# Performance work log

Measured on AMD Instinct MI355X. Metric: run time of the kernel, lower is better.

Reference implementation:

```python
import jax, jax.numpy as jnp
import numpy as np

ALPHA = 1.0

def setup_inputs() -> dict:
    key = jax.random.key(0)
    k1, k2 = jax.random.split(key)
    x = jax.random.normal(k1, (65536, 256), dtype=jnp.float32)
    clusters = jax.random.normal(k2, (512, 256), dtype=jnp.float32)
    return {"x": x, "clusters": clusters}

def reference(x, clusters):
    # squared L2 distance without materializing [B, K, D] broadcasts:
    # d[b,k] = |x_b|^2 + |c_k|^2 - 2 x_b . c_k
    x_sq = jnp.sum(x * x, axis=1, keepdims=True)            # [B, 1]
    c_sq = jnp.sum(clusters * clusters, axis=1)[None, :]    # [1, K]
    cross = jnp.einsum('bd,kd->bk', x, clusters)            # [B, K]
    d = x_sq + c_sq - 2.0 * cross                           # [B, K]
    # Student-t kernel soft assignment
    q = (1.0 + d / ALPHA) ** (-(ALPHA + 1.0) / 2.0)
    q = q / jnp.sum(q, axis=1, keepdims=True)
    return q
```

## Files before the change

kernel.cpp:

```cpp
#include <hip/hip_runtime.h>
#include <hip/hip_bf16.h>

typedef __attribute__((ext_vector_type(8))) short bf16x8;
typedef __attribute__((ext_vector_type(4))) float f32x4;

#define K_DIM 256
#define N_DIM 512
#define BM 32
#define M_DIM 65536

__device__ __forceinline__ unsigned short f2bf(float f) {
    unsigned int u = __float_as_uint(f);
    unsigned int r = (u + 0x7fffu + ((u >> 16) & 1u)) >> 16;
    return (unsigned short)r;
}

__device__ __forceinline__ void gload_lds16(const unsigned short* g, unsigned short* l) {
    __builtin_amdgcn_global_load_lds(
        (const __attribute__((address_space(1))) void*)g,
        (__attribute__((address_space(3))) void*)l, 16, 0, 0);
}

__global__ __launch_bounds__(256) void prep_clusters(
        const float* __restrict__ clusters,
        unsigned short* __restrict__ cba,
        float* __restrict__ csq) {
    const int row = blockIdx.x;
    const int t = threadIdx.x;
    const float v = clusters[row * K_DIM + t];
    const int wc = row >> 6, n = (row >> 4) & 3, r = row & 15;
    const int ks = t >> 5, kh = (t >> 3) & 3, ko = t & 7;
    cba[(size_t)wc * 16384 + ks * 2048 + n * 512 + (kh * 16 + r) * 8 + ko] = f2bf(v);
    float s = v * v;
    #pragma unroll
    for (int m = 1; m < 64; m <<= 1) s += __shfl_xor(s, m);
    __shared__ float red[4];
    if ((t & 63) == 0) red[t >> 6] = s;
    __syncthreads();
    if (t == 0) csq[row] = red[0] + red[1] + red[2] + red[3];
}

__global__ __launch_bounds__(512, 6) void cluster_q(
        const float* __restrict__ x,
        const unsigned short* __restrict__ cba,
        const float* __restrict__ csq,
        float* __restrict__ out) {
    __shared__ __align__(16) unsigned short xa[BM * K_DIM];
    __shared__ __align__(16) unsigned short bB[8 * 2048];
    __shared__ float xsq[BM];
    __shared__ __align__(16) float csql[N_DIM];
    __shared__ float rsum[8][BM];

    const int t = threadIdx.x;
    const int lane = t & 63;
    const int wc = t >> 6;
    const int rowbase = blockIdx.x * BM;

    unsigned short* myB = bB + wc * 2048;
    const unsigned short* gsrc = cba + (size_t)wc * 16384;

    #pragma unroll
    for (int n = 0; n < 4; ++n)
        gload_lds16(gsrc + n * 512 + lane * 8, myB + n * 512);

    if (t < N_DIM) csql[t] = csq[t];

    #pragma unroll
    for (int p = 0; p < 4; ++p) {
        const int row = wc + p * 8;
        const float4 v = reinterpret_cast<const float4*>(
                             x + (size_t)(rowbase + row) * K_DIM)[lane];
        float s = v.x * v.x + v.y * v.y + v.z * v.z + v.w * v.w;
        #pragma unroll
        for (int m = 1; m < 64; m <<= 1) s += __shfl_xor(s, m);
        if (lane == 0) xsq[row] = s;
        const ushort4 pk = make_ushort4(f2bf(v.x), f2bf(v.y), f2bf(v.z), f2bf(v.w));
        const int swz = (lane * 8) ^ ((row & 7) << 4);
        *reinterpret_cast<ushort4*>(reinterpret_cast<char*>(xa) + row * 512 + swz) = pk;
    }
    __syncthreads();

    f32x4 acc[2][4];
    #pragma unroll
    for (int m = 0; m < 2; ++m)
        #pragma unroll
        for (int n = 0; n < 4; ++n)
            acc[m][n] = (f32x4){0.f, 0.f, 0.f, 0.f};

    #pragma unroll
    for (int ks = 0; ks < 8; ++ks) {
        asm volatile("s_waitcnt vmcnt(0)" ::: "memory");
        __builtin_amdgcn_sched_barrier(0);
        bf16x8 a[4];
        #pragma unroll
        for (int n = 0; n < 4; ++n)
            a[n] = *reinterpret_cast<const bf16x8*>(myB + n * 512 + lane * 8);
        const int r0 = (lane & 15);
        const int r1 = 16 + (lane & 15);
        const int c0 = (ks * 64 + (lane >> 4) * 16) ^ ((r0 & 7) << 4);
        const int c1 = (ks * 64 + (lane >> 4) * 16) ^ ((r1 & 7) << 4);
        const bf16x8 xm0 = *reinterpret_cast<const bf16x8*>(
                               reinterpret_cast<const char*>(xa) + r0 * 512 + c0);
        const bf16x8 xm1 = *reinterpret_cast<const bf16x8*>(
                               reinterpret_cast<const char*>(xa) + r1 * 512 + c1);
        asm volatile("s_waitcnt lgkmcnt(0)" ::: "memory");
        __builtin_amdgcn_sched_barrier(0);
        if (ks < 7) {
            #pragma unroll
            for (int n = 0; n < 4; ++n)
                gload_lds16(gsrc + (ks + 1) * 2048 + n * 512 + lane * 8,
                            myB + n * 512);
        }
        __builtin_amdgcn_sched_barrier(0);
        #pragma unroll
        for (int n = 0; n < 4; ++n) {
            acc[0][n] = __builtin_amdgcn_mfma_f32_16x16x32_bf16(a[n], xm0, acc[0][n], 0, 0, 0);
            acc[1][n] = __builtin_amdgcn_mfma_f32_16x16x32_bf16(a[n], xm1, acc[1][n], 0, 0, 0);
        }
    }

    const float4* csql4 = reinterpret_cast<const float4*>(csql);
    float part[2] = {0.f, 0.f};
    #pragma unroll
    for (int m = 0; m < 2; ++m) {
        const float xs1 = 1.f + xsq[m * 16 + (lane & 15)];
        #pragma unroll
        for (int n = 0; n < 4; ++n) {
            const float4 cs = csql4[wc * 16 + n * 4 + (lane >> 4)];
            f32x4 q;
            q[0] = __builtin_amdgcn_rcpf(fmaf(-2.f, acc[m][n][0], xs1 + cs.x));
            q[1] = __builtin_amdgcn_rcpf(fmaf(-2.f, acc[m][n][1], xs1 + cs.y));
            q[2] = __builtin_amdgcn_rcpf(fmaf(-2.f, acc[m][n][2], xs1 + cs.z));
            q[3] = __builtin_amdgcn_rcpf(fmaf(-2.f, acc[m][n][3], xs1 + cs.w));
            acc[m][n] = q;
            part[m] += (q[0] + q[1]) + (q[2] + q[3]);
        }
    }

    #pragma unroll
    for (int m = 0; m < 2; ++m) {
        float s = part[m];
        s += __shfl_xor(s, 16);
        s += __shfl_xor(s, 32);
        if (lane < 16) rsum[wc][m * 16 + lane] = s;
    }
    __syncthreads();

    #pragma unroll
    for (int m = 0; m < 2; ++m) {
        const int b = m * 16 + (lane & 15);
        const float inv = __builtin_amdgcn_rcpf(
            ((rsum[0][b] + rsum[1][b]) + (rsum[2][b] + rsum[3][b])) +
            ((rsum[4][b] + rsum[5][b]) + (rsum[6][b] + rsum[7][b])));
        float* orow = out + (size_t)(rowbase + b) * N_DIM + wc * 64 + (lane >> 4) * 4;
        #pragma unroll
        for (int n = 0; n < 4; ++n) {
            const f32x4 v = acc[m][n];
            float4 st = make_float4(v[0] * inv, v[1] * inv, v[2] * inv, v[3] * inv);
            *reinterpret_cast<float4*>(orow + n * 16) = st;
        }
    }
}

extern "C" void kernel_launch(void* const* d_in, const int* in_sizes, int n_in,
                              void* d_out, int out_size, void* d_ws, size_t ws_size,
                              hipStream_t stream) {
    const float* x        = (const float*)d_in[0];
    const float* clusters = (const float*)d_in[1];
    float* out = (float*)d_out;
    unsigned short* cba = (unsigned short*)d_ws;
    float* csq = (float*)((char*)d_ws + (size_t)N_DIM * K_DIM * 2);
    prep_clusters<<<N_DIM, K_DIM, 0, stream>>>(clusters, cba, csq);
    cluster_q<<<M_DIM / BM, 512, 0, stream>>>(x, cba, csq, out);
}
```

Measured before the change: 60.45 us.

## Keep cluster tiles in registers and loop blocks over row tiles

Each block now loads its wave's full bf16 cluster slice into registers once (breg[8][4]) and then processes eight 32-row tiles in a persistent loop, instead of streaming cluster tiles through LDS for every 32-row block. The x tile for the next iteration is prefetched into registers while the current one computes, and the grid shrinks by a factor of eight. This removes repeated cluster loads and LDS traffic per tile, at the cost of much higher register use (launch bounds drop to 2 blocks per CU) and fewer resident waves to hide store latency.

Measured after the change: 53.38 us. 11.7% less time.

```diff
diff --git a/kernel.cpp b/kernel.cpp
--- a/kernel.cpp
+++ b/kernel.cpp
@@ -8,17 +8,13 @@
 #define N_DIM 512
 #define BM 32
 #define M_DIM 65536
+#define TPB 8
+#define GRID (M_DIM / BM / TPB)
 
 __device__ __forceinline__ unsigned short f2bf(float f) {
     unsigned int u = __float_as_uint(f);
     unsigned int r = (u + 0x7fffu + ((u >> 16) & 1u)) >> 16;
     return (unsigned short)r;
-}
-
-__device__ __forceinline__ void gload_lds16(const unsigned short* g, unsigned short* l) {
-    __builtin_amdgcn_global_load_lds(
-        (const __attribute__((address_space(1))) void*)g,
-        (__attribute__((address_space(3))) void*)l, 16, 0, 0);
 }
 
 __global__ __launch_bounds__(256) void prep_clusters(
@@ -40,13 +36,12 @@
     if (t == 0) csq[row] = red[0] + red[1] + red[2] + red[3];
 }
 
-__global__ __launch_bounds__(512, 6) void cluster_q(
+__global__ __launch_bounds__(512, 2) void cluster_q(
         const float* __restrict__ x,
         const unsigned short* __restrict__ cba,
         const float* __restrict__ csq,
         float* __restrict__ out) {
     __shared__ __align__(16) unsigned short xa[BM * K_DIM];
-    __shared__ __align__(16) unsigned short bB[8 * 2048];
     __shared__ float xsq[BM];
     __shared__ __align__(16) float csql[N_DIM];
     __shared__ float rsum[8][BM];
@@ -54,110 +49,120 @@
     const int t = threadIdx.x;
     const int lane = t & 63;
     const int wc = t >> 6;
-    const int rowbase = blockIdx.x * BM;
 
-    unsigned short* myB = bB + wc * 2048;
     const unsigned short* gsrc = cba + (size_t)wc * 16384;
-
+    bf16x8 breg[8][4];
     #pragma unroll
-    for (int n = 0; n < 4; ++n)
-        gload_lds16(gsrc + n * 512 + lane * 8, myB + n * 512);
-
-    if (t < N_DIM) csql[t] = csq[t];
-
-    #pragma unroll
-    for (int p = 0; p < 4; ++p) {
-        const int row = wc + p * 8;
-        const float4 v = reinterpret_cast<const float4*>(
-                             x + (size_t)(rowbase + row) * K_DIM)[lane];
-        float s = v.x * v.x + v.y * v.y + v.z * v.z + v.w * v.w;
-        #pragma unroll
-        for (int m = 1; m < 64; m <<= 1) s += __shfl_xor(s, m);
-        if (lane == 0) xsq[row] = s;
-        const ushort4 pk = make_ushort4(f2bf(v.x), f2bf(v.y), f2bf(v.z), f2bf(v.w));
-        const int swz = (lane * 8) ^ ((row & 7) << 4);
-        *reinterpret_cast<ushort4*>(reinterpret_cast<char*>(xa) + row * 512 + swz) = pk;
-    }
-    __syncthreads();
-
-    f32x4 acc[2][4];
-    #pragma unroll
-    for (int m = 0; m < 2; ++m)
+    for (int ks = 0; ks < 8; ++ks)
         #pragma unroll
         for (int n = 0; n < 4; ++n)
-            acc[m][n] = (f32x4){0.f, 0.f, 0.f, 0.f};
+            breg[ks][n] = *reinterpret_cast<const bf16x8*>(
+                              gsrc + ks * 2048 + n * 512 + lane * 8);
 
-    #pragma unroll
-    for (int ks = 0; ks < 8; ++ks) {
-        asm volatile("s_waitcnt vmcnt(0)" ::: "memory");
+    csql[t] = csq[t];
+
+    const size_t base = (size_t)blockIdx.x * (TPB * BM);
+
+    float4 xr0, xr1, xr2, xr3;
+    {
+        const float4* xp = reinterpret_cast<const float4*>(x + (base + wc) * K_DIM);
+        xr0 = xp[lane];
+        xr1 = xp[512 + lane];
+        xr2 = xp[1024 + lane];
+        xr3 = xp[1536 + lane];
+    }
+
+    for (int it = 0; it < TPB; ++it) {
+        const size_t rowbase = base + (size_t)it * BM;
+
+        const float4 vv[4] = {xr0, xr1, xr2, xr3};
+        #pragma unroll
+        for (int p = 0; p < 4; ++p) {
+            const int row = wc + p * 8;
+            const float4 v = vv[p];
+            float s = v.x * v.x + v.y * v.y + v.z * v.z + v.w * v.w;
+            #pragma unroll
+            for (int m = 1; m < 64; m <<= 1) s += __shfl_xor(s, m);
+            if (lane == 0) xsq[row] = s;
+            const ushort4 pk = make_ushort4(f2bf(v.x), f2bf(v.y), f2bf(v.z), f2bf(v.w));
+            const int swz = (lane * 8) ^ ((row & 7) << 4);
+            *reinterpret_cast<ushort4*>(reinterpret_cast<char*>(xa) + row * 512 + swz) = pk;
+        }
+        __syncthreads();
+
+        if (it + 1 < TPB) {
+            const float4* xp = reinterpret_cast<const float4*>(
+                                   x + (rowbase + BM + wc) * K_DIM);
+            xr0 = xp[lane];
+            xr1 = xp[512 + lane];
+            xr2 = xp[1024 + lane];
+            xr3 = xp[1536 + lane];
+        }
         __builtin_amdgcn_sched_barrier(0);
-        bf16x8 a[4];
+
+        f32x4 acc[2][4];
         #pragma unroll
-        for (int n = 0; n < 4; ++n)
-            a[n] = *reinterpret_cast<const bf16x8*>(myB + n * 512 + lane * 8);
-        const int r0 = (lane & 15);
-        const int r1 = 16 + (lane & 15);
-        const int c0 = (ks * 64 + (lane >> 4) * 16) ^ ((r0 & 7) << 4);
-        const int c1 = (ks * 64 + (lane >> 4) * 16) ^ ((r1 & 7) << 4);
-        const bf16x8 xm0 = *reinterpret_cast<const bf16x8*>(
-                               reinterpret_cast<const char*>(xa) + r0 * 512 + c0);
-        const bf16x8 xm1 = *reinterpret_cast<const bf16x8*>(
-                               reinterpret_cast<const char*>(xa) + r1 * 512 + c1);
-        asm volatile("s_waitcnt lgkmcnt(0)" ::: "memory");
-        __builtin_amdgcn_sched_barrier(0);
-        if (ks < 7) {
+        for (int m = 0; m < 2; ++m)
             #pragma unroll
             for (int n = 0; n < 4; ++n)
-                gload_lds16(gsrc + (ks + 1) * 2048 + n * 512 + lane * 8,
-                            myB + n * 512);
+                acc[m][n] = (f32x4){0.f, 0.f, 0.f, 0.f};
+
+        #pragma unroll
+        for (int ks = 0; ks < 8; ++ks) {
+            const int r0 = (lane & 15);
+            const int r1 = 16 + (lane & 15);
+            const int c0 = (ks * 64 + (lane >> 4) * 16) ^ ((r0 & 7) << 4);
+            const int c1 = (ks * 64 + (lane >> 4) * 16) ^ ((r1 & 7) << 4);
+            const bf16x8 xm0 = *reinterpret_cast<const bf16x8*>(
+                                   reinterpret_cast<const char*>(xa) + r0 * 512 + c0);
+            const bf16x8 xm1 = *reinterpret_cast<const bf16x8*>(
+                                   reinterpret_cast<const char*>(xa) + r1 * 512 + c1);
+            #pragma unroll
+            for (int n = 0; n < 4; ++n) {
+                acc[0][n] = __builtin_amdgcn_mfma_f32_16x16x32_bf16(breg[ks][n], xm0, acc[0][n], 0, 0, 0);
+                acc[1][n] = __builtin_amdgcn_mfma_f32_16x16x32_bf16(breg[ks][n], xm1, acc[1][n], 0, 0, 0);
+            }
         }
-        __builtin_amdgcn_sched_barrier(0);
+
+        const float4* csql4 = reinterpret_cast<const float4*>(csql);
+        float part[2] = {0.f, 0.f};
         #pragma unroll
-        for (int n = 0; n < 4; ++n) {
-            acc[0][n] = __builtin_amdgcn_mfma_f32_16x16x32_bf16(a[n], xm0, acc[0][n], 0, 0, 0);
-            acc[1][n] = __builtin_amdgcn_mfma_f32_16x16x32_bf16(a[n], xm1, acc[1][n], 0, 0, 0);
+        for (int m = 0; m < 2; ++m) {
+            const float xs1 = 1.f + xsq[m * 16 + (lane & 15)];
+            #pragma unroll
+            for (int n = 0; n < 4; ++n) {
+                const float4 cs = csql4[wc * 16 + n * 4 + (lane >> 4)];
+                f32x4 q;
+                q[0] = __builtin_amdgcn_rcpf(fmaf(-2.f, acc[m][n][0], xs1 + cs.x));
+                q[1] = __builtin_amdgcn_rcpf(fmaf(-2.f, acc[m][n][1], xs1 + cs.y));
+                q[2] = __builtin_amdgcn_rcpf(fmaf(-2.f, acc[m][n][2], xs1 + cs.z));
+                q[3] = __builtin_amdgcn_rcpf(fmaf(-2.f, acc[m][n][3], xs1 + cs.w));
+                acc[m][n] = q;
+                part[m] += (q[0] + q[1]) + (q[2] + q[3]);
+            }
         }
-    }
+        #pragma unroll
+        for (int m = 0; m < 2; ++m) {
+            float s = part[m];
+            s += __shfl_xor(s, 16);
+            s += __shfl_xor(s, 32);
+            if (lane < 16) rsum[wc][m * 16 + lane] = s;
+        }
+        __syncthreads();
 
-    const float4* csql4 = reinterpret_cast<const float4*>(csql);
-    float part[2] = {0.f, 0.f};
-    #pragma unroll
-    for (int m = 0; m < 2; ++m) {
-        const float xs1 = 1.f + xsq[m * 16 + (lane & 15)];
         #pragma unroll
-        for (int n = 0; n < 4; ++n) {
-            const float4 cs = csql4[wc * 16 + n * 4 + (lane >> 4)];
-            f32x4 q;
-            q[0] = __builtin_amdgcn_rcpf(fmaf(-2.f, acc[m][n][0], xs1 + cs.x));
-            q[1] = __builtin_amdgcn_rcpf(fmaf(-2.f, acc[m][n][1], xs1 + cs.y));
-            q[2] = __builtin_amdgcn_rcpf(fmaf(-2.f, acc[m][n][2], xs1 + cs.z));
-            q[3] = __builtin_amdgcn_rcpf(fmaf(-2.f, acc[m][n][3], xs1 + cs.w));
-            acc[m][n] = q;
-            part[m] += (q[0] + q[1]) + (q[2] + q[3]);
-        }
-    }
-
-    #pragma unroll
-    for (int m = 0; m < 2; ++m) {
-        float s = part[m];
-        s += __shfl_xor(s, 16);
-        s += __shfl_xor(s, 32);
-        if (lane < 16) rsum[wc][m * 16 + lane] = s;
-    }
-    __syncthreads();
-
-    #pragma unroll
-    for (int m = 0; m < 2; ++m) {
-        const int b = m * 16 + (lane & 15);
-        const float inv = __builtin_amdgcn_rcpf(
-            ((rsum[0][b] + rsum[1][b]) + (rsum[2][b] + rsum[3][b])) +
-            ((rsum[4][b] + rsum[5][b]) + (rsum[6][b] + rsum[7][b])));
-        float* orow = out + (size_t)(rowbase + b) * N_DIM + wc * 64 + (lane >> 4) * 4;
-        #pragma unroll
-        for (int n = 0; n < 4; ++n) {
-            const f32x4 v = acc[m][n];
-            float4 st = make_float4(v[0] * inv, v[1] * inv, v[2] * inv, v[3] * inv);
-            *reinterpret_cast<float4*>(orow + n * 16) = st;
+        for (int m = 0; m < 2; ++m) {
+            const int b = m * 16 + (lane & 15);
+            const float inv = __builtin_amdgcn_rcpf(
+                ((rsum[0][b] + rsum[1][b]) + (rsum[2][b] + rsum[3][b])) +
+                ((rsum[4][b] + rsum[5][b]) + (rsum[6][b] + rsum[7][b])));
+            float* orow = out + (rowbase + b) * N_DIM + wc * 64 + (lane >> 4) * 4;
+            #pragma unroll
+            for (int n = 0; n < 4; ++n) {
+                const f32x4 v = acc[m][n];
+                float4 st = make_float4(v[0] * inv, v[1] * inv, v[2] * inv, v[3] * inv);
+                *reinterpret_cast<float4*>(orow + n * 16) = st;
+            }
         }
     }
 }
@@ -171,5 +176,5 @@
     unsigned short* cba = (unsigned short*)d_ws;
     float* csq = (float*)((char*)d_ws + (size_t)N_DIM * K_DIM * 2);
     prep_clusters<<<N_DIM, K_DIM, 0, stream>>>(clusters, cba, csq);
-    cluster_q<<<M_DIM / BM, 512, 0, stream>>>(x, cba, csq, out);
+    cluster_q<<<GRID, 512, 0, stream>>>(x, cba, csq, out);
 }
```
